# Kernel optimization log

Hardware: AMD Instinct MI355X
Metric: run time of the kernel (lower is better)

Reference implementation:

```python
import jax, jax.numpy as jnp
import numpy as np

N_NODES = 100000
N_EDGES = 1600000
IN_CH, HID_CH, OUT_CH = 128, 128, 64


def setup_inputs() -> dict:
    key = jax.random.key(0)
    ks = jax.random.split(key, 9)
    x = jax.random.normal(ks[0], (N_NODES, IN_CH), dtype=jnp.float32)
    edge_index = jax.random.randint(ks[1], (2, N_EDGES), 0, N_NODES, dtype=jnp.int64)
    def glorot(k, shape):
        fan_in = shape[1]
        return jax.random.normal(k, shape, dtype=jnp.float32) / jnp.sqrt(jnp.float32(fan_in))
    return {
        "x": x,
        "edge_index": edge_index,
        "W1_l": glorot(ks[2], (HID_CH, IN_CH)),
        "W1_r": glorot(ks[3], (HID_CH, IN_CH)),
        "b1": jnp.zeros((HID_CH,), jnp.float32),
        "W2_l": glorot(ks[4], (HID_CH, HID_CH)),
        "W2_r": glorot(ks[5], (HID_CH, HID_CH)),
        "b2": jnp.zeros((HID_CH,), jnp.float32),
        "W3_l": glorot(ks[6], (OUT_CH, HID_CH)),
        "W3_r": glorot(ks[7], (OUT_CH, HID_CH)),
        "b3": jnp.zeros((OUT_CH,), jnp.float32),
    }


def _sage_conv(x, src, dst, W_l, W_r, b):
    # PyG SAGEConv (aggr='mean', root_weight=True): out = lin_l(mean_j x_j) + lin_r(x_i)
    n = x.shape[0]
    msg = x[src]                                            # [E, C] gather at source
    agg = jax.ops.segment_sum(msg, dst, num_segments=n)     # [N, C] scatter-sum at dest
    cnt = jax.ops.segment_sum(jnp.ones((src.shape[0],), x.dtype), dst, num_segments=n)
    mean = agg / jnp.maximum(cnt, 1.0)[:, None]             # zero-in-degree nodes -> 0
    return mean @ W_l.T + x @ W_r.T + b


def reference(x, edge_index, W1_l, W1_r, b1, W2_l, W2_r, b2, W3_l, W3_r, b3):
    src, dst = edge_index[0], edge_index[1]
    h = jax.nn.relu(_sage_conv(x, src, dst, W1_l, W1_r, b1))
    # F.dropout with training=False is identity (eval mode)
    h = jax.nn.relu(_sage_conv(h, src, dst, W2_l, W2_r, b2))
    return _sage_conv(h, src, dst, W3_l, W3_r, b3)
```

## Files before the change

### kernel.cpp

```cpp
#include <hip/hip_runtime.h>
#include <hip/hip_bf16.h>
#include <cstddef>
#include <cstdint>

#define NBLK(n, b) (((n) + (b) - 1) / (b))

typedef __attribute__((ext_vector_type(8))) short short8;
typedef __attribute__((ext_vector_type(4))) float f32x4;

__device__ inline unsigned short f2bf(float f) {
  union { float f; unsigned u; } v; v.f = f;
  unsigned u = v.u;
  u += 0x7FFFu + ((u >> 16) & 1u);
  return (unsigned short)(u >> 16);
}
__device__ inline float bflo(unsigned u) { union { unsigned u; float f; } v; v.u = u << 16; return v.f; }
__device__ inline float bfhi(unsigned u) { union { unsigned u; float f; } v; v.u = u & 0xFFFF0000u; return v.f; }

#define BSHIFT 9
#define BSIZE 512
#define CAPSHIFT 14
#define CAP 16384
#define ECHUNK 4096

__global__ __launch_bounds__(256) void k_setup(
    const float* __restrict__ x, unsigned* __restrict__ xb, int N,
    const float* __restrict__ W1l, const float* __restrict__ W1r, unsigned short* __restrict__ Wb1,
    const float* __restrict__ W2l, const float* __restrict__ W2r, unsigned short* __restrict__ Wb2,
    const float* __restrict__ W3l, const float* __restrict__ W3r, unsigned short* __restrict__ Wb3,
    const void* __restrict__ edges, int* __restrict__ bucketCursor,
    unsigned* __restrict__ bucketed, int E, int NB) {
  __shared__ int h[1024];
  __shared__ int base2[1024];
  int t = threadIdx.x;
  int b = blockIdx.x;
  int gCast = (N * 64 + 255) >> 8;
  if (b < gCast) {
    int i = b * 256 + t;
    if (i < N * 64) {
      float2 v = *(const float2*)(x + (size_t)i * 2);
      xb[i] = (unsigned)f2bf(v.x) | ((unsigned)f2bf(v.y) << 16);
    }
    return;
  }
  b -= gCast;
  if (b < 320) {
    int ii = b * 256 + t;
    const float *Wl, *Wr; unsigned short* Wb;
    if (ii < 128 * 256) { Wl = W1l; Wr = W1r; Wb = Wb1; }
    else if (ii < 256 * 256) { Wl = W2l; Wr = W2r; Wb = Wb2; ii -= 128 * 256; }
    else { Wl = W3l; Wr = W3r; Wb = Wb3; ii -= 256 * 256; }
    int nrow = ii >> 8, k = ii & 255;
    float v = (k < 128) ? Wr[nrow * 128 + k] : Wl[nrow * 128 + (k - 128)];
    Wb[ii] = f2bf(v);
    return;
  }
  b -= 320;

  const unsigned* e32 = (const unsigned*)edges;
  int is64 = 1;
#pragma unroll
  for (int i = 0; i < 16; ++i)
    if (e32[2 * i + 1] != 0u) is64 = 0;

  for (int i = t; i < NB; i += 256) h[i] = 0;
  __syncthreads();
  int base_e = b * ECHUNK;
  unsigned key[16];
  int bkt[16];
#pragma unroll
  for (int k = 0; k < 16; ++k) {
    int e = base_e + k * 256 + t;
    bkt[k] = -1;
    if (e < E) {
      int s, d;
      if (is64) {
        s = (int)((const long long*)edges)[e];
        d = (int)((const long long*)edges)[(size_t)E + e];
      } else {
        s = ((const int*)edges)[e];
        d = ((const int*)edges)[(size_t)E + e];
      }
      bkt[k] = d >> BSHIFT;
      key[k] = (unsigned)s | ((unsigned)(d & (BSIZE - 1)) << 17);
      atomicAdd(&h[bkt[k]], 1);
    }
  }
  __syncthreads();
  for (int i = t; i < NB; i += 256) {
    int c = h[i];
    base2[i] = c ? atomicAdd(&bucketCursor[i], c) : 0;
    h[i] = 0;
  }
  __syncthreads();
#pragma unroll
  for (int k = 0; k < 16; ++k) {
    if (bkt[k] >= 0) {
      int r = atomicAdd(&h[bkt[k]], 1);
      int pos = base2[bkt[k]] + r;
      if (pos < CAP)
        bucketed[((size_t)bkt[k] << CAPSHIFT) + pos] = key[k];
    }
  }
}

__global__ __launch_bounds__(256) void k_csr(const unsigned* __restrict__ bucketed,
                                             const int* __restrict__ bucketCursor,
                                             int* __restrict__ rowStart, int* __restrict__ deg,
                                             int* __restrict__ srcSorted, int N, int NB) {
  __shared__ int h[512];
  __shared__ int excl[512];
  __shared__ int sd[256];
  int b = blockIdx.x;
  int t = threadIdx.x;
  int nodeBase = b << BSHIFT;
  int nNode = min(BSIZE, N - nodeBase);
  int cnt = min(bucketCursor[b], CAP);
  size_t s0 = (size_t)b << CAPSHIFT;
  h[t * 2] = 0; h[t * 2 + 1] = 0;
  __syncthreads();
  for (int i = t; i < cnt; i += 256) {
    int ld = bucketed[s0 + i] >> 17;
    atomicAdd(&h[ld], 1);
  }
  __syncthreads();
  int a0 = h[t * 2], a1 = h[t * 2 + 1];
  int s = a0 + a1;
  sd[t] = s;
  __syncthreads();
  for (int off = 1; off < 256; off <<= 1) {
    int xv = (t >= off) ? sd[t - off] : 0;
    __syncthreads();
    sd[t] += xv;
    __syncthreads();
  }
  int run = sd[t] - s;
  excl[t * 2] = run;
  excl[t * 2 + 1] = run + a0;
  if (t * 2 < nNode) {
    rowStart[nodeBase + t * 2] = (int)s0 + run;
    deg[nodeBase + t * 2] = a0;
  }
  if (t * 2 + 1 < nNode) {
    rowStart[nodeBase + t * 2 + 1] = (int)s0 + run + a0;
    deg[nodeBase + t * 2 + 1] = a1;
  }
  h[t * 2] = 0; h[t * 2 + 1] = 0;
  __syncthreads();
  for (int i = t; i < cnt; i += 256) {
    unsigned u = bucketed[s0 + i];
    int ld = u >> 17;
    int r = atomicAdd(&h[ld], 1);
    srcSorted[s0 + excl[ld] + r] = (int)(u & 0x1FFFFu);
  }
}

__global__ void k_aggregate(const unsigned* __restrict__ in, const int* __restrict__ rowStart,
                            const int* __restrict__ deg, const int* __restrict__ srcs,
                            unsigned* __restrict__ mean, int n) {
  int lane = threadIdx.x & 63;
  int w = threadIdx.x >> 6;
  int node = blockIdx.x * 4 + w;
  if (node >= n) return;
  int r0 = rowStart[node];
  int dg = deg[node];
  int r1 = r0 + dg;
  int sub = lane & 15;
  int eg = lane >> 4;
  float acc[8];
#pragma unroll
  for (int k = 0; k < 8; ++k) acc[k] = 0.f;

  for (int base = r0; base < r1; base += 64) {
    int e = base + lane;
    int sv = (e < r1) ? srcs[e] : 0;
    int cnt = min(64, r1 - base);
    int j = 0;
    for (; j + 16 <= cnt; j += 16) {
      int s0 = __shfl(sv, j + eg);
      int s1 = __shfl(sv, j + 4 + eg);
      int s2 = __shfl(sv, j + 8 + eg);
      int s3 = __shfl(sv, j + 12 + eg);
      uint4 u0 = *(const uint4*)(in + (size_t)s0 * 64 + sub * 4);
      uint4 u1 = *(const uint4*)(in + (size_t)s1 * 64 + sub * 4);
      uint4 u2 = *(const uint4*)(in + (size_t)s2 * 64 + sub * 4);
      uint4 u3 = *(const uint4*)(in + (size_t)s3 * 64 + sub * 4);
      acc[0] += bflo(u0.x); acc[1] += bfhi(u0.x);
      acc[2] += bflo(u0.y); acc[3] += bfhi(u0.y);
      acc[4] += bflo(u0.z); acc[5] += bfhi(u0.z);
      acc[6] += bflo(u0.w); acc[7] += bfhi(u0.w);
      acc[0] += bflo(u1.x); acc[1] += bfhi(u1.x);
      acc[2] += bflo(u1.y); acc[3] += bfhi(u1.y);
      acc[4] += bflo(u1.z); acc[5] += bfhi(u1.z);
      acc[6] += bflo(u1.w); acc[7] += bfhi(u1.w);
      acc[0] += bflo(u2.x); acc[1] += bfhi(u2.x);
      acc[2] += bflo(u2.y); acc[3] += bfhi(u2.y);
      acc[4] += bflo(u2.z); acc[5] += bfhi(u2.z);
      acc[6] += bflo(u2.w); acc[7] += bfhi(u2.w);
      acc[0] += bflo(u3.x); acc[1] += bfhi(u3.x);
      acc[2] += bflo(u3.y); acc[3] += bfhi(u3.y);
      acc[4] += bflo(u3.z); acc[5] += bfhi(u3.z);
      acc[6] += bflo(u3.w); acc[7] += bfhi(u3.w);
    }
    for (; j + 8 <= cnt; j += 8) {
      int s0 = __shfl(sv, j + eg);
      int s1 = __shfl(sv, j + 4 + eg);
      uint4 u0 = *(const uint4*)(in + (size_t)s0 * 64 + sub * 4);
      uint4 u1 = *(const uint4*)(in + (size_t)s1 * 64 + sub * 4);
      acc[0] += bflo(u0.x); acc[1] += bfhi(u0.x);
      acc[2] += bflo(u0.y); acc[3] += bfhi(u0.y);
      acc[4] += bflo(u0.z); acc[5] += bfhi(u0.z);
      acc[6] += bflo(u0.w); acc[7] += bfhi(u0.w);
      acc[0] += bflo(u1.x); acc[1] += bfhi(u1.x);
      acc[2] += bflo(u1.y); acc[3] += bfhi(u1.y);
      acc[4] += bflo(u1.z); acc[5] += bfhi(u1.z);
      acc[6] += bflo(u1.w); acc[7] += bfhi(u1.w);
    }
    for (; j < cnt; j += 4) {
      int jj = j + eg;
      int s = __shfl(sv, jj);
      if (jj < cnt) {
        uint4 u = *(const uint4*)(in + (size_t)s * 64 + sub * 4);
        acc[0] += bflo(u.x); acc[1] += bfhi(u.x);
        acc[2] += bflo(u.y); acc[3] += bfhi(u.y);
        acc[4] += bflo(u.z); acc[5] += bfhi(u.z);
        acc[6] += bflo(u.w); acc[7] += bfhi(u.w);
      }
    }
  }

#pragma unroll
  for (int k = 0; k < 8; ++k) {
    acc[k] += __shfl_down(acc[k], 32);
    acc[k] += __shfl_down(acc[k], 16);
  }
  if (eg == 0) {
    float sc = 1.0f / (float)max(dg, 1);
    uint4 o;
    o.x = (unsigned)f2bf(acc[0] * sc) | ((unsigned)f2bf(acc[1] * sc) << 16);
    o.y = (unsigned)f2bf(acc[2] * sc) | ((unsigned)f2bf(acc[3] * sc) << 16);
    o.z = (unsigned)f2bf(acc[4] * sc) | ((unsigned)f2bf(acc[5] * sc) << 16);
    o.w = (unsigned)f2bf(acc[6] * sc) | ((unsigned)f2bf(acc[7] * sc) << 16);
    *(uint4*)(mean + (size_t)node * 64 + sub * 4) = o;
  }
}

template <int H, bool RELU, bool BF16OUT>
__global__ __launch_bounds__(256) void k_gemm(
    const unsigned short* __restrict__ selfB, const unsigned short* __restrict__ meanB,
    const unsigned short* __restrict__ Wb, const float* __restrict__ bias,
    void* __restrict__ outp, int n) {
  constexpr int TN = H / 32;
  int lane = threadIdx.x & 63;
  int w = threadIdx.x >> 6;
  int wr = w & 1, wc = w >> 1;
  int nodeBase = blockIdx.x * 128 + wr * 64;
  int colBase = wc * (H / 2);
  int l15 = lane & 15, quad = lane >> 4;

  f32x4 acc[4][TN];
#pragma unroll
  for (int t = 0; t < 4; ++t)
#pragma unroll
    for (int j = 0; j < TN; ++j) acc[t][j] = (f32x4){0.f, 0.f, 0.f, 0.f};

#pragma unroll
  for (int c = 0; c < 8; ++c) {
    const unsigned short* A = (c < 4) ? selfB : meanB;
    int ko = (c & 3) * 32 + quad * 8;
    short8 af[4], bfr[TN];
#pragma unroll
    for (int t = 0; t < 4; ++t) {
      int row = nodeBase + t * 16 + l15;
      row = min(row, n - 1);
      af[t] = *(const short8*)(A + (size_t)row * 128 + ko);
    }
#pragma unroll
    for (int j = 0; j < TN; ++j) {
      int cn = colBase + j * 16 + l15;
      bfr[j] = *(const short8*)(Wb + (size_t)cn * 256 + c * 32 + quad * 8);
    }
#pragma unroll
    for (int t = 0; t < 4; ++t)
#pragma unroll
      for (int j = 0; j < TN; ++j)
        acc[t][j] = __builtin_amdgcn_mfma_f32_16x16x32_bf16(af[t], bfr[j], acc[t][j], 0, 0, 0);
  }

#pragma unroll
  for (int j = 0; j < TN; ++j) {
    int col = colBase + j * 16 + l15;
    float bv = bias[col];
#pragma unroll
    for (int t = 0; t < 4; ++t) {
#pragma unroll
      for (int r = 0; r < 4; ++r) {
        int row = nodeBase + t * 16 + quad * 4 + r;
        if (row < n) {
          float v = acc[t][j][r] + bv;
          if (RELU) v = fmaxf(v, 0.f);
          if (BF16OUT) ((unsigned short*)outp)[(size_t)row * H + col] = f2bf(v);
          else ((float*)outp)[(size_t)row * H + col] = v;
        }
      }
    }
  }
}


extern "C" void kernel_launch(void* const* d_in, const int* in_sizes, int n_in,
                              void* d_out, int out_size, void* d_ws, size_t ws_size,
                              hipStream_t stream) {
  (void)n_in; (void)out_size; (void)ws_size;
  const float* x = (const float*)d_in[0];
  const void* edges = d_in[1];
  const float* W1l = (const float*)d_in[2];
  const float* W1r = (const float*)d_in[3];
  const float* b1 = (const float*)d_in[4];
  const float* W2l = (const float*)d_in[5];
  const float* W2r = (const float*)d_in[6];
  const float* b2 = (const float*)d_in[7];
  const float* W3l = (const float*)d_in[8];
  const float* W3r = (const float*)d_in[9];
  const float* b3 = (const float*)d_in[10];
  float* out = (float*)d_out;

  const int N = in_sizes[0] / 128;
  const int E = in_sizes[1] / 2;
  const int NB = (N + BSIZE - 1) >> BSHIFT;

  char* ws = (char*)d_ws;
  size_t off = 0;
  auto alloc = [&](size_t bytes) -> char* {
    char* p = ws + off;
    off = (off + bytes + 255) & ~(size_t)255;
    return p;
  };
  int* bucketCursor = (int*)alloc((size_t)NB * 4);
  unsigned* bucketed = (unsigned*)alloc((size_t)NB * CAP * 4);
  int* rowStart = (int*)alloc((size_t)N * 4);
  int* deg = (int*)alloc((size_t)N * 4);
  int* srcSorted = (int*)alloc((size_t)NB * CAP * 4);
  unsigned short* xb = (unsigned short*)alloc((size_t)N * 128 * 2);
  unsigned short* mean = (unsigned short*)alloc((size_t)N * 128 * 2);
  unsigned short* h1 = (unsigned short*)alloc((size_t)N * 128 * 2);
  unsigned short* h2 = (unsigned short*)alloc((size_t)N * 128 * 2);
  unsigned short* Wb1 = (unsigned short*)alloc(128 * 256 * 2);
  unsigned short* Wb2 = (unsigned short*)alloc(128 * 256 * 2);
  unsigned short* Wb3 = (unsigned short*)alloc(64 * 256 * 2);

  int gE = NBLK(E, ECHUNK);
  int gSetup = NBLK(N * 64, 256) + 320 + gE;

  hipMemsetAsync(bucketCursor, 0, (size_t)NB * 4, stream);
  k_setup<<<gSetup, 256, 0, stream>>>(x, (unsigned*)xb, N,
                                      W1l, W1r, Wb1, W2l, W2r, Wb2, W3l, W3r, Wb3,
                                      edges, bucketCursor, bucketed, E, NB);
  k_csr<<<NB, 256, 0, stream>>>(bucketed, bucketCursor, rowStart, deg, srcSorted, N, NB);

  int gAgg = NBLK(N, 4);
  int gGemm = NBLK(N, 128);

  k_aggregate<<<gAgg, 256, 0, stream>>>((const unsigned*)xb, rowStart, deg, srcSorted, (unsigned*)mean, N);
  k_gemm<128, true, true><<<gGemm, 256, 0, stream>>>(xb, mean, Wb1, b1, h1, N);
  k_aggregate<<<gAgg, 256, 0, stream>>>((const unsigned*)h1, rowStart, deg, srcSorted, (unsigned*)mean, N);
  k_gemm<128, true, true><<<gGemm, 256, 0, stream>>>(h1, mean, Wb2, b2, h2, N);
  k_aggregate<<<gAgg, 256, 0, stream>>>((const unsigned*)h2, rowStart, deg, srcSorted, (unsigned*)mean, N);
  k_gemm<64, false, false><<<gGemm, 256, 0, stream>>>(h2, mean, Wb3, b3, out, N);
}
```

Measured before the change: 462.5 us.

## Fuse mean aggregation into GEMM and aggregate projected features in layer three

Layers one and two now aggregate neighbour means for 128 nodes per block into shared memory, then run the MFMA GEMM directly from LDS. This removes the global mean buffer round trip and two kernel launches. Layer three applies W3_l before aggregation, using linearity of the mean, so the gather moves 64-wide rows instead of 128-wide ones; the final kernel fuses that aggregation with the root GEMM. The trade-off is fewer blocks (one per 128 nodes) with serial per-wave node loops, which may reduce latency hiding in the gather phase, and y3 is rounded to bf16 before averaging.

After: 607.5 us. 31.3% more time.

```diff
diff --git a/kernel.cpp b/kernel.cpp
--- a/kernel.cpp
+++ b/kernel.cpp
@@ -155,140 +155,152 @@
   }
 }
 
-__global__ void k_aggregate(const unsigned* __restrict__ in, const int* __restrict__ rowStart,
-                            const int* __restrict__ deg, const int* __restrict__ srcs,
-                            unsigned* __restrict__ mean, int n) {
+template <bool RELU>
+__global__ __launch_bounds__(256, 3) void k_fused128(
+    const unsigned* __restrict__ in,
+    const int* __restrict__ rowStart, const int* __restrict__ deg,
+    const int* __restrict__ srcs,
+    const unsigned short* __restrict__ Wb,
+    const float* __restrict__ bias,
+    unsigned short* __restrict__ outp,
+    int n) {
+  __shared__ unsigned meanL[128][68];
   int lane = threadIdx.x & 63;
   int w = threadIdx.x >> 6;
-  int node = blockIdx.x * 4 + w;
-  if (node >= n) return;
-  int r0 = rowStart[node];
-  int dg = deg[node];
-  int r1 = r0 + dg;
-  int sub = lane & 15;
-  int eg = lane >> 4;
-  float acc[8];
-#pragma unroll
-  for (int k = 0; k < 8; ++k) acc[k] = 0.f;
-
-  for (int base = r0; base < r1; base += 64) {
-    int e = base + lane;
-    int sv = (e < r1) ? srcs[e] : 0;
-    int cnt = min(64, r1 - base);
-    int j = 0;
-    for (; j + 16 <= cnt; j += 16) {
-      int s0 = __shfl(sv, j + eg);
-      int s1 = __shfl(sv, j + 4 + eg);
-      int s2 = __shfl(sv, j + 8 + eg);
-      int s3 = __shfl(sv, j + 12 + eg);
-      uint4 u0 = *(const uint4*)(in + (size_t)s0 * 64 + sub * 4);
-      uint4 u1 = *(const uint4*)(in + (size_t)s1 * 64 + sub * 4);
-      uint4 u2 = *(const uint4*)(in + (size_t)s2 * 64 + sub * 4);
-      uint4 u3 = *(const uint4*)(in + (size_t)s3 * 64 + sub * 4);
-      acc[0] += bflo(u0.x); acc[1] += bfhi(u0.x);
-      acc[2] += bflo(u0.y); acc[3] += bfhi(u0.y);
-      acc[4] += bflo(u0.z); acc[5] += bfhi(u0.z);
-      acc[6] += bflo(u0.w); acc[7] += bfhi(u0.w);
-      acc[0] += bflo(u1.x); acc[1] += bfhi(u1.x);
-      acc[2] += bflo(u1.y); acc[3] += bfhi(u1.y);
-      acc[4] += bflo(u1.z); acc[5] += bfhi(u1.z);
-      acc[6] += bflo(u1.w); acc[7] += bfhi(u1.w);
-      acc[0] += bflo(u2.x); acc[1] += bfhi(u2.x);
-      acc[2] += bflo(u2.y); acc[3] += bfhi(u2.y);
-      acc[4] += bflo(u2.z); acc[5] += bfhi(u2.z);
-      acc[6] += bflo(u2.w); acc[7] += bfhi(u2.w);
-      acc[0] += bflo(u3.x); acc[1] += bfhi(u3.x);
-      acc[2] += bflo(u3.y); acc[3] += bfhi(u3.y);
-      acc[4] += bflo(u3.z); acc[5] += bfhi(u3.z);
-      acc[6] += bflo(u3.w); acc[7] += bfhi(u3.w);
-    }
-    for (; j + 8 <= cnt; j += 8) {
-      int s0 = __shfl(sv, j + eg);
-      int s1 = __shfl(sv, j + 4 + eg);
-      uint4 u0 = *(const uint4*)(in + (size_t)s0 * 64 + sub * 4);
-      uint4 u1 = *(const uint4*)(in + (size_t)s1 * 64 + sub * 4);
-      acc[0] += bflo(u0.x); acc[1] += bfhi(u0.x);
-      acc[2] += bflo(u0.y); acc[3] += bfhi(u0.y);
-      acc[4] += bflo(u0.z); acc[5] += bfhi(u0.z);
-      acc[6] += bflo(u0.w); acc[7] += bfhi(u0.w);
-      acc[0] += bflo(u1.x); acc[1] += bfhi(u1.x);
-      acc[2] += bflo(u1.y); acc[3] += bfhi(u1.y);
-      acc[4] += bflo(u1.z); acc[5] += bfhi(u1.z);
-      acc[6] += bflo(u1.w); acc[7] += bfhi(u1.w);
-    }
-    for (; j < cnt; j += 4) {
-      int jj = j + eg;
-      int s = __shfl(sv, jj);
-      if (jj < cnt) {
-        uint4 u = *(const uint4*)(in + (size_t)s * 64 + sub * 4);
-        acc[0] += bflo(u.x); acc[1] += bfhi(u.x);
-        acc[2] += bflo(u.y); acc[3] += bfhi(u.y);
-        acc[4] += bflo(u.z); acc[5] += bfhi(u.z);
-        acc[6] += bflo(u.w); acc[7] += bfhi(u.w);
-      }
-    }
-  }
-
-#pragma unroll
-  for (int k = 0; k < 8; ++k) {
-    acc[k] += __shfl_down(acc[k], 32);
-    acc[k] += __shfl_down(acc[k], 16);
-  }
-  if (eg == 0) {
-    float sc = 1.0f / (float)max(dg, 1);
-    uint4 o;
-    o.x = (unsigned)f2bf(acc[0] * sc) | ((unsigned)f2bf(acc[1] * sc) << 16);
-    o.y = (unsigned)f2bf(acc[2] * sc) | ((unsigned)f2bf(acc[3] * sc) << 16);
-    o.z = (unsigned)f2bf(acc[4] * sc) | ((unsigned)f2bf(acc[5] * sc) << 16);
-    o.w = (unsigned)f2bf(acc[6] * sc) | ((unsigned)f2bf(acc[7] * sc) << 16);
-    *(uint4*)(mean + (size_t)node * 64 + sub * 4) = o;
-  }
-}
-
-template <int H, bool RELU, bool BF16OUT>
-__global__ __launch_bounds__(256) void k_gemm(
-    const unsigned short* __restrict__ selfB, const unsigned short* __restrict__ meanB,
-    const unsigned short* __restrict__ Wb, const float* __restrict__ bias,
-    void* __restrict__ outp, int n) {
-  constexpr int TN = H / 32;
-  int lane = threadIdx.x & 63;
-  int w = threadIdx.x >> 6;
+  int blockBase = blockIdx.x * 128;
+
+  {
+    int sub = lane & 15, eg = lane >> 4;
+    for (int it = 0; it < 32; ++it) {
+      int local = w * 32 + it;
+      int node = blockBase + local;
+      float acc[8];
+#pragma unroll
+      for (int k = 0; k < 8; ++k) acc[k] = 0.f;
+      int dg = 0;
+      if (node < n) {
+        int r0 = rowStart[node];
+        dg = deg[node];
+        int r1 = r0 + dg;
+        for (int base = r0; base < r1; base += 64) {
+          int e = base + lane;
+          int sv = (e < r1) ? srcs[e] : 0;
+          int cnt = min(64, r1 - base);
+          int j = 0;
+          for (; j + 16 <= cnt; j += 16) {
+            int s0 = __shfl(sv, j + eg);
+            int s1 = __shfl(sv, j + 4 + eg);
+            int s2 = __shfl(sv, j + 8 + eg);
+            int s3 = __shfl(sv, j + 12 + eg);
+            uint4 u0 = *(const uint4*)(in + (size_t)s0 * 64 + sub * 4);
+            uint4 u1 = *(const uint4*)(in + (size_t)s1 * 64 + sub * 4);
+            uint4 u2 = *(const uint4*)(in + (size_t)s2 * 64 + sub * 4);
+            uint4 u3 = *(const uint4*)(in + (size_t)s3 * 64 + sub * 4);
+            acc[0] += bflo(u0.x); acc[1] += bfhi(u0.x);
+            acc[2] += bflo(u0.y); acc[3] += bfhi(u0.y);
+            acc[4] += bflo(u0.z); acc[5] += bfhi(u0.z);
+            acc[6] += bflo(u0.w); acc[7] += bfhi(u0.w);
+            acc[0] += bflo(u1.x); acc[1] += bfhi(u1.x);
+            acc[2] += bflo(u1.y); acc[3] += bfhi(u1.y);
+            acc[4] += bflo(u1.z); acc[5] += bfhi(u1.z);
+            acc[6] += bflo(u1.w); acc[7] += bfhi(u1.w);
+            acc[0] += bflo(u2.x); acc[1] += bfhi(u2.x);
+            acc[2] += bflo(u2.y); acc[3] += bfhi(u2.y);
+            acc[4] += bflo(u2.z); acc[5] += bfhi(u2.z);
+            acc[6] += bflo(u2.w); acc[7] += bfhi(u2.w);
+            acc[0] += bflo(u3.x); acc[1] += bfhi(u3.x);
+            acc[2] += bflo(u3.y); acc[3] += bfhi(u3.y);
+            acc[4] += bflo(u3.z); acc[5] += bfhi(u3.z);
+            acc[6] += bflo(u3.w); acc[7] += bfhi(u3.w);
+          }
+          for (; j + 8 <= cnt; j += 8) {
+            int s0 = __shfl(sv, j + eg);
+            int s1 = __shfl(sv, j + 4 + eg);
+            uint4 u0 = *(const uint4*)(in + (size_t)s0 * 64 + sub * 4);
+            uint4 u1 = *(const uint4*)(in + (size_t)s1 * 64 + sub * 4);
+            acc[0] += bflo(u0.x); acc[1] += bfhi(u0.x);
+            acc[2] += bflo(u0.y); acc[3] += bfhi(u0.y);
+            acc[4] += bflo(u0.z); acc[5] += bfhi(u0.z);
+            acc[6] += bflo(u0.w); acc[7] += bfhi(u0.w);
+            acc[0] += bflo(u1.x); acc[1] += bfhi(u1.x);
+            acc[2] += bflo(u1.y); acc[3] += bfhi(u1.y);
+            acc[4] += bflo(u1.z); acc[5] += bfhi(u1.z);
+            acc[6] += bflo(u1.w); acc[7] += bfhi(u1.w);
+          }
+          for (; j < cnt; j += 4) {
+            int jj = j + eg;
+            int s = __shfl(sv, jj);
+            if (jj < cnt) {
+              uint4 u = *(const uint4*)(in + (size_t)s * 64 + sub * 4);
+              acc[0] += bflo(u.x); acc[1] += bfhi(u.x);
+              acc[2] += bflo(u.y); acc[3] += bfhi(u.y);
+              acc[4] += bflo(u.z); acc[5] += bfhi(u.z);
+              acc[6] += bflo(u.w); acc[7] += bfhi(u.w);
+            }
+          }
+        }
+      }
+#pragma unroll
+      for (int k = 0; k < 8; ++k) {
+        acc[k] += __shfl_down(acc[k], 32);
+        acc[k] += __shfl_down(acc[k], 16);
+      }
+      if (eg == 0) {
+        float sc = 1.0f / (float)max(dg, 1);
+        uint4 o;
+        o.x = (unsigned)f2bf(acc[0] * sc) | ((unsigned)f2bf(acc[1] * sc) << 16);
+        o.y = (unsigned)f2bf(acc[2] * sc) | ((unsigned)f2bf(acc[3] * sc) << 16);
+        o.z = (unsigned)f2bf(acc[4] * sc) | ((unsigned)f2bf(acc[5] * sc) << 16);
+        o.w = (unsigned)f2bf(acc[6] * sc) | ((unsigned)f2bf(acc[7] * sc) << 16);
+        *(uint4*)&meanL[local][sub * 4] = o;
+      }
+    }
+  }
+  __syncthreads();
+
+  const unsigned short* selfB = (const unsigned short*)in;
   int wr = w & 1, wc = w >> 1;
-  int nodeBase = blockIdx.x * 128 + wr * 64;
-  int colBase = wc * (H / 2);
+  int nodeBase = blockBase + wr * 64;
+  int colBase = wc * 64;
   int l15 = lane & 15, quad = lane >> 4;
 
-  f32x4 acc[4][TN];
+  f32x4 acc[4][4];
 #pragma unroll
   for (int t = 0; t < 4; ++t)
 #pragma unroll
-    for (int j = 0; j < TN; ++j) acc[t][j] = (f32x4){0.f, 0.f, 0.f, 0.f};
+    for (int j = 0; j < 4; ++j) acc[t][j] = (f32x4){0.f, 0.f, 0.f, 0.f};
 
 #pragma unroll
   for (int c = 0; c < 8; ++c) {
-    const unsigned short* A = (c < 4) ? selfB : meanB;
     int ko = (c & 3) * 32 + quad * 8;
-    short8 af[4], bfr[TN];
-#pragma unroll
-    for (int t = 0; t < 4; ++t) {
-      int row = nodeBase + t * 16 + l15;
-      row = min(row, n - 1);
-      af[t] = *(const short8*)(A + (size_t)row * 128 + ko);
-    }
-#pragma unroll
-    for (int j = 0; j < TN; ++j) {
+    short8 af[4], bfr[4];
+    if (c < 4) {
+#pragma unroll
+      for (int t = 0; t < 4; ++t) {
+        int row = min(nodeBase + t * 16 + l15, n - 1);
+        af[t] = *(const short8*)(selfB + (size_t)row * 128 + ko);
+      }
+    } else {
+#pragma unroll
+      for (int t = 0; t < 4; ++t) {
+        int lrow = wr * 64 + t * 16 + l15;
+        af[t] = *(const short8*)((const unsigned short*)&meanL[lrow][0] + ko);
+      }
+    }
+#pragma unroll
+    for (int j = 0; j < 4; ++j) {
       int cn = colBase + j * 16 + l15;
       bfr[j] = *(const short8*)(Wb + (size_t)cn * 256 + c * 32 + quad * 8);
     }
 #pragma unroll
     for (int t = 0; t < 4; ++t)
 #pragma unroll
-      for (int j = 0; j < TN; ++j)
+      for (int j = 0; j < 4; ++j)
         acc[t][j] = __builtin_amdgcn_mfma_f32_16x16x32_bf16(af[t], bfr[j], acc[t][j], 0, 0, 0);
   }
 
 #pragma unroll
-  for (int j = 0; j < TN; ++j) {
+  for (int j = 0; j < 4; ++j) {
     int col = colBase + j * 16 + l15;
     float bv = bias[col];
 #pragma unroll
@@ -299,9 +311,178 @@
         if (row < n) {
           float v = acc[t][j][r] + bv;
           if (RELU) v = fmaxf(v, 0.f);
-          if (BF16OUT) ((unsigned short*)outp)[(size_t)row * H + col] = f2bf(v);
-          else ((float*)outp)[(size_t)row * H + col] = v;
+          outp[(size_t)row * 128 + col] = f2bf(v);
         }
+      }
+    }
+  }
+}
+
+__global__ __launch_bounds__(256, 4) void k_gemm_y3(
+    const unsigned short* __restrict__ A,
+    const unsigned short* __restrict__ Wb3,
+    unsigned short* __restrict__ y3, int n) {
+  int lane = threadIdx.x & 63;
+  int w = threadIdx.x >> 6;
+  int wr = w & 1, wc = w >> 1;
+  int nodeBase = blockIdx.x * 128 + wr * 64;
+  int colBase = wc * 32;
+  int l15 = lane & 15, quad = lane >> 4;
+  f32x4 acc[4][2];
+#pragma unroll
+  for (int t = 0; t < 4; ++t)
+#pragma unroll
+    for (int j = 0; j < 2; ++j) acc[t][j] = (f32x4){0.f, 0.f, 0.f, 0.f};
+#pragma unroll
+  for (int c = 0; c < 4; ++c) {
+    int ko = c * 32 + quad * 8;
+    short8 af[4], bfr[2];
+#pragma unroll
+    for (int t = 0; t < 4; ++t) {
+      int row = min(nodeBase + t * 16 + l15, n - 1);
+      af[t] = *(const short8*)(A + (size_t)row * 128 + ko);
+    }
+#pragma unroll
+    for (int j = 0; j < 2; ++j) {
+      int cn = colBase + j * 16 + l15;
+      bfr[j] = *(const short8*)(Wb3 + (size_t)cn * 256 + 128 + c * 32 + quad * 8);
+    }
+#pragma unroll
+    for (int t = 0; t < 4; ++t)
+#pragma unroll
+      for (int j = 0; j < 2; ++j)
+        acc[t][j] = __builtin_amdgcn_mfma_f32_16x16x32_bf16(af[t], bfr[j], acc[t][j], 0, 0, 0);
+  }
+#pragma unroll
+  for (int j = 0; j < 2; ++j) {
+    int col = colBase + j * 16 + l15;
+#pragma unroll
+    for (int t = 0; t < 4; ++t) {
+#pragma unroll
+      for (int r = 0; r < 4; ++r) {
+        int row = nodeBase + t * 16 + quad * 4 + r;
+        if (row < n) y3[(size_t)row * 64 + col] = f2bf(acc[t][j][r]);
+      }
+    }
+  }
+}
+
+__global__ __launch_bounds__(256, 3) void k_final(
+    const unsigned* __restrict__ y3,
+    const unsigned short* __restrict__ selfB,
+    const int* __restrict__ rowStart, const int* __restrict__ deg,
+    const int* __restrict__ srcs,
+    const unsigned short* __restrict__ Wb3,
+    const float* __restrict__ bias,
+    float* __restrict__ outp, int n) {
+  __shared__ float meanL[128][72];
+  int lane = threadIdx.x & 63;
+  int w = threadIdx.x >> 6;
+  int blockBase = blockIdx.x * 128;
+
+  {
+    int sub = lane & 7, eg = lane >> 3;
+    for (int it = 0; it < 32; ++it) {
+      int local = w * 32 + it;
+      int node = blockBase + local;
+      float acc[8];
+#pragma unroll
+      for (int k = 0; k < 8; ++k) acc[k] = 0.f;
+      int dg = 0;
+      if (node < n) {
+        int r0 = rowStart[node];
+        dg = deg[node];
+        int r1 = r0 + dg;
+        for (int base = r0; base < r1; base += 64) {
+          int e = base + lane;
+          int sv = (e < r1) ? srcs[e] : 0;
+          int cnt = min(64, r1 - base);
+          int j = 0;
+          for (; j + 16 <= cnt; j += 16) {
+            int s0 = __shfl(sv, j + eg);
+            int s1 = __shfl(sv, j + 8 + eg);
+            uint4 u0 = *(const uint4*)(y3 + (size_t)s0 * 32 + sub * 4);
+            uint4 u1 = *(const uint4*)(y3 + (size_t)s1 * 32 + sub * 4);
+            acc[0] += bflo(u0.x); acc[1] += bfhi(u0.x);
+            acc[2] += bflo(u0.y); acc[3] += bfhi(u0.y);
+            acc[4] += bflo(u0.z); acc[5] += bfhi(u0.z);
+            acc[6] += bflo(u0.w); acc[7] += bfhi(u0.w);
+            acc[0] += bflo(u1.x); acc[1] += bfhi(u1.x);
+            acc[2] += bflo(u1.y); acc[3] += bfhi(u1.y);
+            acc[4] += bflo(u1.z); acc[5] += bfhi(u1.z);
+            acc[6] += bflo(u1.w); acc[7] += bfhi(u1.w);
+          }
+          for (; j < cnt; j += 8) {
+            int jj = j + eg;
+            int s = __shfl(sv, jj);
+            if (jj < cnt) {
+              uint4 u = *(const uint4*)(y3 + (size_t)s * 32 + sub * 4);
+              acc[0] += bflo(u.x); acc[1] += bfhi(u.x);
+              acc[2] += bflo(u.y); acc[3] += bfhi(u.y);
+              acc[4] += bflo(u.z); acc[5] += bfhi(u.z);
+              acc[6] += bflo(u.w); acc[7] += bfhi(u.w);
+            }
+          }
+        }
+      }
+#pragma unroll
+      for (int k = 0; k < 8; ++k) {
+        acc[k] += __shfl_down(acc[k], 32);
+        acc[k] += __shfl_down(acc[k], 16);
+        acc[k] += __shfl_down(acc[k], 8);
+      }
+      if (eg == 0) {
+        float sc = 1.0f / (float)max(dg, 1);
+        float4 o0 = make_float4(acc[0] * sc, acc[1] * sc, acc[2] * sc, acc[3] * sc);
+        float4 o1 = make_float4(acc[4] * sc, acc[5] * sc, acc[6] * sc, acc[7] * sc);
+        *(float4*)&meanL[local][sub * 8] = o0;
+        *(float4*)&meanL[local][sub * 8 + 4] = o1;
+      }
+    }
+  }
+  __syncthreads();
+
+  int wr = w & 1, wc = w >> 1;
+  int nodeBase = blockBase + wr * 64;
+  int colBase = wc * 32;
+  int l15 = lane & 15, quad = lane >> 4;
+  f32x4 acc[4][2];
+#pragma unroll
+  for (int t = 0; t < 4; ++t)
+#pragma unroll
+    for (int j = 0; j < 2; ++j) acc[t][j] = (f32x4){0.f, 0.f, 0.f, 0.f};
+#pragma unroll
+  for (int c = 0; c < 4; ++c) {
+    int ko = c * 32 + quad * 8;
+    short8 af[4], bfr[2];
+#pragma unroll
+    for (int t = 0; t < 4; ++t) {
+      int row = min(nodeBase + t * 16 + l15, n - 1);
+      af[t] = *(const short8*)(selfB + (size_t)row * 128 + ko);
+    }
+#pragma unroll
+    for (int j = 0; j < 2; ++j) {
+      int cn = colBase + j * 16 + l15;
+      bfr[j] = *(const short8*)(Wb3 + (size_t)cn * 256 + c * 32 + quad * 8);
+    }
+#pragma unroll
+    for (int t = 0; t < 4; ++t)
+#pragma unroll
+      for (int j = 0; j < 2; ++j)
+        acc[t][j] = __builtin_amdgcn_mfma_f32_16x16x32_bf16(af[t], bfr[j], acc[t][j], 0, 0, 0);
+  }
+#pragma unroll
+  for (int j = 0; j < 2; ++j) {
+    int col = colBase + j * 16 + l15;
+    float bv = bias[col];
+#pragma unroll
+    for (int t = 0; t < 4; ++t) {
+#pragma unroll
+      for (int r = 0; r < 4; ++r) {
+        int lrow = wr * 64 + t * 16 + quad * 4 + r;
+        int row = blockBase + lrow;
+        if (row < n)
+          outp[(size_t)row * 64 + col] = acc[t][j][r] + meanL[lrow][col] + bv;
       }
     }
   }
@@ -342,15 +523,16 @@
   int* deg = (int*)alloc((size_t)N * 4);
   int* srcSorted = (int*)alloc((size_t)NB * CAP * 4);
   unsigned short* xb = (unsigned short*)alloc((size_t)N * 128 * 2);
-  unsigned short* mean = (unsigned short*)alloc((size_t)N * 128 * 2);
   unsigned short* h1 = (unsigned short*)alloc((size_t)N * 128 * 2);
   unsigned short* h2 = (unsigned short*)alloc((size_t)N * 128 * 2);
+  unsigned short* y3 = (unsigned short*)alloc((size_t)N * 64 * 2);
   unsigned short* Wb1 = (unsigned short*)alloc(128 * 256 * 2);
   unsigned short* Wb2 = (unsigned short*)alloc(128 * 256 * 2);
   unsigned short* Wb3 = (unsigned short*)alloc(64 * 256 * 2);
 
   int gE = NBLK(E, ECHUNK);
   int gSetup = NBLK(N * 64, 256) + 320 + gE;
+  int gF = NBLK(N, 128);
 
   hipMemsetAsync(bucketCursor, 0, (size_t)NB * 4, stream);
   k_setup<<<gSetup, 256, 0, stream>>>(x, (unsigned*)xb, N,
@@ -358,13 +540,11 @@
                                       edges, bucketCursor, bucketed, E, NB);
   k_csr<<<NB, 256, 0, stream>>>(bucketed, bucketCursor, rowStart, deg, srcSorted, N, NB);
 
-  int gAgg = NBLK(N, 4);
-  int gGemm = NBLK(N, 128);
-
-  k_aggregate<<<gAgg, 256, 0, stream>>>((const unsigned*)xb, rowStart, deg, srcSorted, (unsigned*)mean, N);
-  k_gemm<128, true, true><<<gGemm, 256, 0, stream>>>(xb, mean, Wb1, b1, h1, N);
-  k_aggregate<<<gAgg, 256, 0, stream>>>((const unsigned*)h1, rowStart, deg, srcSorted, (unsigned*)mean, N);
-  k_gemm<128, true, true><<<gGemm, 256, 0, stream>>>(h1, mean, Wb2, b2, h2, N);
-  k_aggregate<<<gAgg, 256, 0, stream>>>((const unsigned*)h2, rowStart, deg, srcSorted, (unsigned*)mean, N);
-  k_gemm<64, false, false><<<gGemm, 256, 0, stream>>>(h2, mean, Wb3, b3, out, N);
-}
+  k_fused128<true><<<gF, 256, 0, stream>>>((const unsigned*)xb, rowStart, deg, srcSorted,
+                                           Wb1, b1, h1, N);
+  k_fused128<true><<<gF, 256, 0, stream>>>((const unsigned*)h1, rowStart, deg, srcSorted,
+                                           Wb2, b2, h2, N);
+  k_gemm_y3<<<gF, 256, 0, stream>>>(h2, Wb3, y3, N);
+  k_final<<<gF, 256, 0, stream>>>((const unsigned*)y3, h2, rowStart, deg, srcSorted,
+                                  Wb3, b3, out, N);
+}
```

## Reorder layer-3 to transform before aggregating and split setup kernel

Applied to the files above, without the earlier changes.

For the final layer, the code now multiplies h2 by W3_l and W3_r first, producing a 64-wide bf16 projected tensor y3 alongside the root term. It then mean-aggregates y3 over neighbours and adds the result into the fp32 output. This halves the gather width of the last aggregation, which is the memory-bound step. The fused setup kernel is also split into separate cast and scatter kernels, and the edge chunk per block is halved. Rounding y3 to bf16 before summation changes numerics slightly.

New measurement: 461.6 us. Within noise of the previous version (-0.2%).

```diff
diff --git a/kernel.cpp b/kernel.cpp
--- a/kernel.cpp
+++ b/kernel.cpp
@@ -21,17 +21,13 @@
 #define BSIZE 512
 #define CAPSHIFT 14
 #define CAP 16384
-#define ECHUNK 4096
-
-__global__ __launch_bounds__(256) void k_setup(
+#define ECHUNK 2048
+
+__global__ __launch_bounds__(256) void k_cast(
     const float* __restrict__ x, unsigned* __restrict__ xb, int N,
     const float* __restrict__ W1l, const float* __restrict__ W1r, unsigned short* __restrict__ Wb1,
     const float* __restrict__ W2l, const float* __restrict__ W2r, unsigned short* __restrict__ Wb2,
-    const float* __restrict__ W3l, const float* __restrict__ W3r, unsigned short* __restrict__ Wb3,
-    const void* __restrict__ edges, int* __restrict__ bucketCursor,
-    unsigned* __restrict__ bucketed, int E, int NB) {
-  __shared__ int h[1024];
-  __shared__ int base2[1024];
+    const float* __restrict__ W3l, const float* __restrict__ W3r, unsigned short* __restrict__ Wb3) {
   int t = threadIdx.x;
   int b = blockIdx.x;
   int gCast = (N * 64 + 255) >> 8;
@@ -44,18 +40,23 @@
     return;
   }
   b -= gCast;
-  if (b < 320) {
-    int ii = b * 256 + t;
-    const float *Wl, *Wr; unsigned short* Wb;
-    if (ii < 128 * 256) { Wl = W1l; Wr = W1r; Wb = Wb1; }
-    else if (ii < 256 * 256) { Wl = W2l; Wr = W2r; Wb = Wb2; ii -= 128 * 256; }
-    else { Wl = W3l; Wr = W3r; Wb = Wb3; ii -= 256 * 256; }
-    int nrow = ii >> 8, k = ii & 255;
-    float v = (k < 128) ? Wr[nrow * 128 + k] : Wl[nrow * 128 + (k - 128)];
-    Wb[ii] = f2bf(v);
-    return;
-  }
-  b -= 320;
+  int ii = b * 256 + t;
+  const float *Wl, *Wr; unsigned short* Wb;
+  if (ii < 128 * 256) { Wl = W1l; Wr = W1r; Wb = Wb1; }
+  else if (ii < 256 * 256) { Wl = W2l; Wr = W2r; Wb = Wb2; ii -= 128 * 256; }
+  else { Wl = W3l; Wr = W3r; Wb = Wb3; ii -= 256 * 256; }
+  int nrow = ii >> 8, k = ii & 255;
+  float v = (k < 128) ? Wr[nrow * 128 + k] : Wl[nrow * 128 + (k - 128)];
+  Wb[ii] = f2bf(v);
+}
+
+__global__ __launch_bounds__(256) void k_scatter(
+    const void* __restrict__ edges, int* __restrict__ bucketCursor,
+    unsigned* __restrict__ bucketed, int E, int NB) {
+  __shared__ int h[1024];
+  __shared__ int base2[1024];
+  int t = threadIdx.x;
+  int b = blockIdx.x;
 
   const unsigned* e32 = (const unsigned*)edges;
   int is64 = 1;
@@ -66,10 +67,10 @@
   for (int i = t; i < NB; i += 256) h[i] = 0;
   __syncthreads();
   int base_e = b * ECHUNK;
-  unsigned key[16];
-  int bkt[16];
-#pragma unroll
-  for (int k = 0; k < 16; ++k) {
+  unsigned key[8];
+  int bkt[8];
+#pragma unroll
+  for (int k = 0; k < 8; ++k) {
     int e = base_e + k * 256 + t;
     bkt[k] = -1;
     if (e < E) {
@@ -94,7 +95,7 @@
   }
   __syncthreads();
 #pragma unroll
-  for (int k = 0; k < 16; ++k) {
+  for (int k = 0; k < 8; ++k) {
     if (bkt[k] >= 0) {
       int r = atomicAdd(&h[bkt[k]], 1);
       int pos = base2[bkt[k]] + r;
@@ -271,8 +272,7 @@
     short8 af[4], bfr[TN];
 #pragma unroll
     for (int t = 0; t < 4; ++t) {
-      int row = nodeBase + t * 16 + l15;
-      row = min(row, n - 1);
+      int row = min(nodeBase + t * 16 + l15, n - 1);
       af[t] = *(const short8*)(A + (size_t)row * 128 + ko);
     }
 #pragma unroll
@@ -304,6 +304,128 @@
         }
       }
     }
+  }
+}
+
+__global__ __launch_bounds__(256) void k_gemm3_both(
+    const unsigned short* __restrict__ A,
+    const unsigned short* __restrict__ Wb3,
+    const float* __restrict__ bias,
+    float* __restrict__ outp, unsigned short* __restrict__ y3, int n) {
+  int lane = threadIdx.x & 63;
+  int w = threadIdx.x >> 6;
+  int wr = w & 1, wc = w >> 1;
+  int nodeBase = blockIdx.x * 128 + wr * 64;
+  int l15 = lane & 15, quad = lane >> 4;
+  int woff = wc ? 128 : 0;
+  f32x4 acc[4][4];
+#pragma unroll
+  for (int t = 0; t < 4; ++t)
+#pragma unroll
+    for (int j = 0; j < 4; ++j) acc[t][j] = (f32x4){0.f, 0.f, 0.f, 0.f};
+#pragma unroll
+  for (int c = 0; c < 4; ++c) {
+    int ko = c * 32 + quad * 8;
+    short8 af[4], bfr[4];
+#pragma unroll
+    for (int t = 0; t < 4; ++t) {
+      int row = min(nodeBase + t * 16 + l15, n - 1);
+      af[t] = *(const short8*)(A + (size_t)row * 128 + ko);
+    }
+#pragma unroll
+    for (int j = 0; j < 4; ++j) {
+      int cn = j * 16 + l15;
+      bfr[j] = *(const short8*)(Wb3 + (size_t)cn * 256 + woff + c * 32 + quad * 8);
+    }
+#pragma unroll
+    for (int t = 0; t < 4; ++t)
+#pragma unroll
+      for (int j = 0; j < 4; ++j)
+        acc[t][j] = __builtin_amdgcn_mfma_f32_16x16x32_bf16(af[t], bfr[j], acc[t][j], 0, 0, 0);
+  }
+#pragma unroll
+  for (int j = 0; j < 4; ++j) {
+    int col = j * 16 + l15;
+    float bv = wc ? 0.f : bias[col];
+#pragma unroll
+    for (int t = 0; t < 4; ++t) {
+#pragma unroll
+      for (int r = 0; r < 4; ++r) {
+        int row = nodeBase + t * 16 + quad * 4 + r;
+        if (row < n) {
+          float v = acc[t][j][r] + bv;
+          if (wc) y3[(size_t)row * 64 + col] = f2bf(v);
+          else outp[(size_t)row * 64 + col] = v;
+        }
+      }
+    }
+  }
+}
+
+__global__ void k_agg64_add(const unsigned* __restrict__ y3, const int* __restrict__ rowStart,
+                            const int* __restrict__ deg, const int* __restrict__ srcs,
+                            float* __restrict__ outp, int n) {
+  int lane = threadIdx.x & 63;
+  int w = threadIdx.x >> 6;
+  int node = blockIdx.x * 4 + w;
+  if (node >= n) return;
+  int dg = deg[node];
+  if (dg == 0) return;
+  int r0 = rowStart[node];
+  int r1 = r0 + dg;
+  int sub = lane & 7;
+  int eg = lane >> 3;
+  float acc[8];
+#pragma unroll
+  for (int k = 0; k < 8; ++k) acc[k] = 0.f;
+
+  for (int base = r0; base < r1; base += 64) {
+    int e = base + lane;
+    int sv = (e < r1) ? srcs[e] : 0;
+    int cnt = min(64, r1 - base);
+    int j = 0;
+    for (; j + 16 <= cnt; j += 16) {
+      int s0 = __shfl(sv, j + eg);
+      int s1 = __shfl(sv, j + 8 + eg);
+      uint4 u0 = *(const uint4*)(y3 + (size_t)s0 * 32 + sub * 4);
+      uint4 u1 = *(const uint4*)(y3 + (size_t)s1 * 32 + sub * 4);
+      acc[0] += bflo(u0.x); acc[1] += bfhi(u0.x);
+      acc[2] += bflo(u0.y); acc[3] += bfhi(u0.y);
+      acc[4] += bflo(u0.z); acc[5] += bfhi(u0.z);
+      acc[6] += bflo(u0.w); acc[7] += bfhi(u0.w);
+      acc[0] += bflo(u1.x); acc[1] += bfhi(u1.x);
+      acc[2] += bflo(u1.y); acc[3] += bfhi(u1.y);
+      acc[4] += bflo(u1.z); acc[5] += bfhi(u1.z);
+      acc[6] += bflo(u1.w); acc[7] += bfhi(u1.w);
+    }
+    for (; j < cnt; j += 8) {
+      int jj = j + eg;
+      int s = __shfl(sv, jj);
+      if (jj < cnt) {
+        uint4 u = *(const uint4*)(y3 + (size_t)s * 32 + sub * 4);
+        acc[0] += bflo(u.x); acc[1] += bfhi(u.x);
+        acc[2] += bflo(u.y); acc[3] += bfhi(u.y);
+        acc[4] += bflo(u.z); acc[5] += bfhi(u.z);
+        acc[6] += bflo(u.w); acc[7] += bfhi(u.w);
+      }
+    }
+  }
+
+#pragma unroll
+  for (int k = 0; k < 8; ++k) {
+    acc[k] += __shfl_down(acc[k], 32);
+    acc[k] += __shfl_down(acc[k], 16);
+    acc[k] += __shfl_down(acc[k], 8);
+  }
+  if (eg == 0) {
+    float sc = 1.0f / (float)dg;
+    float* op = outp + (size_t)node * 64 + sub * 8;
+    float4 a = *(float4*)op;
+    float4 b = *(float4*)(op + 4);
+    a.x += acc[0] * sc; a.y += acc[1] * sc; a.z += acc[2] * sc; a.w += acc[3] * sc;
+    b.x += acc[4] * sc; b.y += acc[5] * sc; b.z += acc[6] * sc; b.w += acc[7] * sc;
+    *(float4*)op = a;
+    *(float4*)(op + 4) = b;
   }
 }
 
@@ -345,26 +467,26 @@
   unsigned short* mean = (unsigned short*)alloc((size_t)N * 128 * 2);
   unsigned short* h1 = (unsigned short*)alloc((size_t)N * 128 * 2);
   unsigned short* h2 = (unsigned short*)alloc((size_t)N * 128 * 2);
+  unsigned short* y3 = (unsigned short*)alloc((size_t)N * 64 * 2);
   unsigned short* Wb1 = (unsigned short*)alloc(128 * 256 * 2);
   unsigned short* Wb2 = (unsigned short*)alloc(128 * 256 * 2);
   unsigned short* Wb3 = (unsigned short*)alloc(64 * 256 * 2);
 
+  int gCast = NBLK(N * 64, 256) + 320;
   int gE = NBLK(E, ECHUNK);
-  int gSetup = NBLK(N * 64, 256) + 320 + gE;
-
-  hipMemsetAsync(bucketCursor, 0, (size_t)NB * 4, stream);
-  k_setup<<<gSetup, 256, 0, stream>>>(x, (unsigned*)xb, N,
-                                      W1l, W1r, Wb1, W2l, W2r, Wb2, W3l, W3r, Wb3,
-                                      edges, bucketCursor, bucketed, E, NB);
-  k_csr<<<NB, 256, 0, stream>>>(bucketed, bucketCursor, rowStart, deg, srcSorted, N, NB);
-
   int gAgg = NBLK(N, 4);
   int gGemm = NBLK(N, 128);
+
+  hipMemsetAsync(bucketCursor, 0, (size_t)NB * 4, stream);
+  k_cast<<<gCast, 256, 0, stream>>>(x, (unsigned*)xb, N,
+                                    W1l, W1r, Wb1, W2l, W2r, Wb2, W3l, W3r, Wb3);
+  k_scatter<<<gE, 256, 0, stream>>>(edges, bucketCursor, bucketed, E, NB);
+  k_csr<<<NB, 256, 0, stream>>>(bucketed, bucketCursor, rowStart, deg, srcSorted, N, NB);
 
   k_aggregate<<<gAgg, 256, 0, stream>>>((const unsigned*)xb, rowStart, deg, srcSorted, (unsigned*)mean, N);
   k_gemm<128, true, true><<<gGemm, 256, 0, stream>>>(xb, mean, Wb1, b1, h1, N);
   k_aggregate<<<gAgg, 256, 0, stream>>>((const unsigned*)h1, rowStart, deg, srcSorted, (unsigned*)mean, N);
   k_gemm<128, true, true><<<gGemm, 256, 0, stream>>>(h1, mean, Wb2, b2, h2, N);
-  k_aggregate<<<gAgg, 256, 0, stream>>>((const unsigned*)h2, rowStart, deg, srcSorted, (unsigned*)mean, N);
-  k_gemm<64, false, false><<<gGemm, 256, 0, stream>>>(h2, mean, Wb3, b3, out, N);
-}
+  k_gemm3_both<<<gGemm, 256, 0, stream>>>(h2, Wb3, b3, out, y3, N);
+  k_agg64_add<<<gAgg, 256, 0, stream>>>((const unsigned*)y3, rowStart, deg, srcSorted, out, N);
+}
```
